# Kernel optimization log

Hardware: AMD Instinct MI355X
Metric: run time of the kernel (lower is better)

## Reference

```python
import jax, jax.numpy as jnp
import numpy as np

N = 200000      # query points
D_IN = 3        # coordinate dims
H = 256         # hidden features
L = 4           # hidden layers (between first and last Perceptron)
S = 8           # n_series == out_features


def setup_inputs() -> dict:
    key = jax.random.key(0)
    ks = jax.random.split(key, 7)
    coords = jax.random.normal(ks[0], (N, D_IN), dtype=jnp.float32)
    # Stacked per-series weights (all series share shapes; original loads the
    # same checkpoint into each, but we use independent random params).
    scale0 = 1.0 / np.sqrt(D_IN)
    scaleh = 1.0 / np.sqrt(H)
    W0 = jax.random.uniform(ks[1], (S, D_IN, H), jnp.float32, -scale0, scale0)
    b0 = jax.random.uniform(ks[2], (S, H), jnp.float32, -scale0, scale0)
    Wh = jax.random.uniform(ks[3], (S, L, H, H), jnp.float32, -scaleh, scaleh)
    bh = jax.random.uniform(ks[4], (S, L, H), jnp.float32, -scaleh, scaleh)
    Wout = jax.random.uniform(ks[5], (S, H, 1), jnp.float32, -scaleh, scaleh)
    bout = jax.random.uniform(ks[6], (S, 1), jnp.float32, -scaleh, scaleh)
    return {"coords": coords, "W0": W0, "b0": b0, "Wh": Wh, "bh": bh,
            "Wout": Wout, "bout": bout}


def reference(coords, W0, b0, Wh, bh, Wout, bout):
    # All S series' MLPs batched into grouped GEMMs (einsum over series axis s).
    # Perceptron = Linear + softplus; last layer is plain Linear.
    h = jax.nn.softplus(jnp.einsum('nd,sdh->snh', coords, W0) + b0[:, None, :])
    for i in range(L):  # small fixed layer count
        h = jax.nn.softplus(
            jnp.einsum('snh,shk->snk', h, Wh[:, i]) + bh[:, i][:, None, :])
    out = jnp.einsum('snh,sho->sno', h, Wout) + bout[:, None, :]  # [S,N,1]
    output = jnp.transpose(out[..., 0], (1, 0))  # concat along dim=1 -> [N,S]
    return (output, coords)
```

## Files before the change

### kernel.cpp

```cpp
#include <hip/hip_runtime.h>
#include <hip/hip_bf16.h>
#include <cstdint>

typedef __attribute__((ext_vector_type(8))) short short8;
typedef __attribute__((ext_vector_type(4))) float float4v;

#define LOG2E 1.44269504088896340736f
#define LN2   0.69314718055994530942f

#if __has_builtin(__builtin_amdgcn_exp2f)
__device__ __forceinline__ float fexp2(float x){ return __builtin_amdgcn_exp2f(x); }
#else
__device__ __forceinline__ float fexp2(float x){ return exp2f(x); }
#endif
#if __has_builtin(__builtin_amdgcn_logf)
__device__ __forceinline__ float flog2(float x){ return __builtin_amdgcn_logf(x); }
#else
__device__ __forceinline__ float flog2(float x){ return log2f(x); }
#endif

__device__ __forceinline__ float softplus_hat(float zh){
  return flog2(1.0f + fexp2(zh));
}

__device__ __forceinline__ unsigned short bf16_trunc(float f){
  return (unsigned short)(__builtin_bit_cast(unsigned int, f) >> 16);
}

#define HSTRIDE 264
#define MISTEP  4288
#define HSIZE   (64 * 264 + 16 * 16)

__global__ void convert_wh(const float* __restrict__ Wh,
                           unsigned short* __restrict__ Wt){
  int e = blockIdx.x * 256 + threadIdx.x;
  int n  = e & 255;
  int k  = (e >> 8) & 255;
  int sl = e >> 16;
  float v = Wh[e];
  __hip_bfloat16 h = __float2bfloat16(v);
  Wt[(sl << 16) + ((k >> 5) << 13) + (n << 5) + (k & 31)] =
      __builtin_bit_cast(unsigned short, h);
}

__device__ __forceinline__ float4v bf16_mfma(short8 a, short8 b, float4v c){
  return __builtin_amdgcn_mfma_f32_16x16x32_bf16(a, b, c, 0, 0, 0);
}

template<int L>
__device__ __forceinline__ void hidden_mfma(
    const unsigned short* __restrict__ bbase0,
    const unsigned short* __restrict__ aptr,
    short8 (&bq)[3][4], float4v (&acc)[4][4])
{
  const unsigned short* bb = bbase0 + L * 65536;
  const unsigned short* bn = bbase0 + (L + 1) * 65536;

  short8 a0[4], a1[4];
  #pragma unroll
  for (int mi = 0; mi < 4; ++mi)
    a0[mi] = *(const short8*)(aptr + mi * MISTEP);

  #pragma unroll
  for (int kb = 0; kb < 8; ++kb) {
    short8* cur = (kb & 1) ? a1 : a0;
    short8* nxt = (kb & 1) ? a0 : a1;
    if (kb < 7) {
      #pragma unroll
      for (int mi = 0; mi < 4; ++mi)
        nxt[mi] = *(const short8*)(aptr + (kb + 1) * 32 + mi * MISTEP);
    }
    const int slot = (8 * L + kb) % 3;
    #pragma unroll
    for (int mi = 0; mi < 4; ++mi)
      #pragma unroll
      for (int ni = 0; ni < 4; ++ni)
        acc[mi][ni] = bf16_mfma(cur[mi], bq[slot][ni], acc[mi][ni]);
    if (kb < 5) {
      #pragma unroll
      for (int ni = 0; ni < 4; ++ni)
        bq[slot][ni] = *(const short8*)(bb + (kb + 3) * 8192 + ni * 512);
    } else if (L < 3) {
      #pragma unroll
      for (int ni = 0; ni < 4; ++ni)
        bq[slot][ni] = *(const short8*)(bn + (kb - 5) * 8192 + ni * 512);
    }
  }
}

__global__ __launch_bounds__(256, 2) void series_mlp(
    const float* __restrict__ coords,
    const float* __restrict__ W0, const float* __restrict__ b0,
    const float* __restrict__ bh,
    const float* __restrict__ Wout, const float* __restrict__ bout,
    const unsigned short* __restrict__ Wt,
    float* __restrict__ out)
{
  __shared__ __align__(16) unsigned short h_lds[HSIZE];
  __shared__ float cbuf[192];

  const int tid  = threadIdx.x;
  const int lane = tid & 63;
  const int wave = tid >> 6;
  const int s    = blockIdx.x & 7;
  const int m0   = (blockIdx.x >> 3) * 64;

  if (tid < 192) cbuf[tid] = coords[m0 * 3 + tid];
  __syncthreads();

  {
    const int c  = tid;
    const float w0 = W0[(s * 3 + 0) * 256 + c] * LOG2E;
    const float w1 = W0[(s * 3 + 1) * 256 + c] * LOG2E;
    const float w2 = W0[(s * 3 + 2) * 256 + c] * LOG2E;
    const float bb = b0[s * 256 + c] * LOG2E;
    const float4v* c4 = (const float4v*)cbuf;
    #pragma unroll
    for (int j = 0; j < 16; ++j) {
      float4v x0 = c4[j * 3 + 0];
      float4v x1 = c4[j * 3 + 1];
      float4v x2 = c4[j * 3 + 2];
      float z0 = fmaf(x0.z, w2, fmaf(x0.y, w1, fmaf(x0.x, w0, bb)));
      float z1 = fmaf(x1.y, w2, fmaf(x1.x, w1, fmaf(x0.w, w0, bb)));
      float z2 = fmaf(x2.x, w2, fmaf(x1.w, w1, fmaf(x1.z, w0, bb)));
      float z3 = fmaf(x2.w, w2, fmaf(x2.z, w1, fmaf(x2.y, w0, bb)));
      h_lds[(4 * j + 0) * HSTRIDE + j * 16 + c] = bf16_trunc(softplus_hat(z0));
      h_lds[(4 * j + 1) * HSTRIDE + j * 16 + c] = bf16_trunc(softplus_hat(z1));
      h_lds[(4 * j + 2) * HSTRIDE + j * 16 + c] = bf16_trunc(softplus_hat(z2));
      h_lds[(4 * j + 3) * HSTRIDE + j * 16 + c] = bf16_trunc(softplus_hat(z3));
    }
  }
  __syncthreads();

  const int colb = (wave << 6) + (lane & 15);
  const int q    = lane >> 4;
  const int lr   = lane & 15;
  const unsigned short* aptr = h_lds + lr * HSTRIDE + (lr >> 2) * 16 + q * 8;
  unsigned short* cptr = h_lds + q * 1072 + colb;

  const unsigned short* bbase0 = Wt + ((s << 2) << 16) + (colb << 5) + (q << 3);

  short8 bq[3][4];
  #pragma unroll
  for (int i = 0; i < 3; ++i)
    #pragma unroll
    for (int ni = 0; ni < 4; ++ni)
      bq[i][ni] = *(const short8*)(bbase0 + i * 8192 + ni * 512);

  float4v acc[4][4];
  const float* bh_s = bh + (s << 10);

  #define HIDDEN_LAYER(L)                                                     \
  {                                                                           \
    float bias[4];                                                            \
    _Pragma("unroll")                                                         \
    for (int ni = 0; ni < 4; ++ni)                                            \
      bias[ni] = bh_s[L * 256 + colb + ni * 16] * LOG2E;                      \
    _Pragma("unroll")                                                         \
    for (int mi = 0; mi < 4; ++mi)                                            \
      _Pragma("unroll")                                                       \
      for (int ni = 0; ni < 4; ++ni)                                          \
        acc[mi][ni] = (float4v){bias[ni], bias[ni], bias[ni], bias[ni]};      \
    hidden_mfma<L>(bbase0, aptr, bq, acc);                                    \
    _Pragma("unroll")                                                         \
    for (int mi = 0; mi < 4; ++mi)                                            \
      _Pragma("unroll")                                                       \
      for (int ni = 0; ni < 4; ++ni) {                                        \
        float4v v = acc[mi][ni];                                              \
        _Pragma("unroll")                                                     \
        for (int r = 0; r < 4; ++r) v[r] = softplus_hat(v[r]);                \
        acc[mi][ni] = v;                                                      \
      }                                                                       \
    __syncthreads();                                                          \
    _Pragma("unroll")                                                         \
    for (int mi = 0; mi < 4; ++mi)                                            \
      _Pragma("unroll")                                                       \
      for (int ni = 0; ni < 4; ++ni) {                                        \
        float4v v = acc[mi][ni];                                              \
        _Pragma("unroll")                                                     \
        for (int r = 0; r < 4; ++r)                                           \
          cptr[mi * MISTEP + r * HSTRIDE + ni * 16] = bf16_trunc(v[r]);       \
      }                                                                       \
    __syncthreads();                                                          \
  }

  HIDDEN_LAYER(0)
  HIDDEN_LAYER(1)
  HIDDEN_LAYER(2)
  #undef HIDDEN_LAYER

  {
    float bias[4];
    #pragma unroll
    for (int ni = 0; ni < 4; ++ni)
      bias[ni] = bh_s[3 * 256 + colb + ni * 16] * LOG2E;
    #pragma unroll
    for (int mi = 0; mi < 4; ++mi)
      #pragma unroll
      for (int ni = 0; ni < 4; ++ni)
        acc[mi][ni] = (float4v){bias[ni], bias[ni], bias[ni], bias[ni]};

    hidden_mfma<3>(bbase0, aptr, bq, acc);

    float wv[4];
    #pragma unroll
    for (int ni = 0; ni < 4; ++ni)
      wv[ni] = Wout[(s << 8) + colb + ni * 16];
    float p[16];
    #pragma unroll
    for (int i = 0; i < 16; ++i) p[i] = 0.f;
    #pragma unroll
    for (int mi = 0; mi < 4; ++mi)
      #pragma unroll
      for (int ni = 0; ni < 4; ++ni) {
        float4v v = acc[mi][ni];
        #pragma unroll
        for (int r = 0; r < 4; ++r)
          p[mi * 4 + r] = fmaf(softplus_hat(v[r]), wv[ni], p[mi * 4 + r]);
      }

    __syncthreads();
    float* red = (float*)h_lds;
    #pragma unroll
    for (int mi = 0; mi < 4; ++mi)
      #pragma unroll
      for (int r = 0; r < 4; ++r) {
        int row = mi * 16 + (q << 2) + r;
        red[row * 68 + (wave << 4) + (lane & 15)] = p[mi * 4 + r];
      }
    __syncthreads();

    if (tid < 64) {
      const float4v* rr = (const float4v*)&red[tid * 68];
      float4v a = rr[0];
      #pragma unroll
      for (int i = 1; i < 16; ++i) {
        float4v b = rr[i];
        a.x += b.x; a.y += b.y; a.z += b.z; a.w += b.w;
      }
      float tot = (a.x + a.y) + (a.z + a.w);
      out[(m0 + tid) * 8 + s] = fmaf(LN2, tot, bout[s]);
    }
  }
}

__global__ __launch_bounds__(256) void series_mlp_slow(
    const float* __restrict__ coords,
    const float* __restrict__ W0, const float* __restrict__ b0,
    const float* __restrict__ Wh, const float* __restrict__ bh,
    const float* __restrict__ Wout, const float* __restrict__ bout,
    float* __restrict__ out)
{
  __shared__ float hh[64 * 256];
  __shared__ float cbuf[192];
  __shared__ float red[256];
  const int tid = threadIdx.x;
  const int s   = blockIdx.y;
  const int m0  = blockIdx.x * 64;

  if (tid < 192) cbuf[tid] = coords[m0 * 3 + tid];
  __syncthreads();
  {
    const float w0 = W0[(s * 3 + 0) * 256 + tid];
    const float w1 = W0[(s * 3 + 1) * 256 + tid];
    const float w2 = W0[(s * 3 + 2) * 256 + tid];
    const float bb = b0[s * 256 + tid];
    for (int m = 0; m < 64; ++m) {
      float z = fmaf(cbuf[m * 3 + 2], w2,
                fmaf(cbuf[m * 3 + 1], w1,
                fmaf(cbuf[m * 3 + 0], w0, bb)));
      hh[m * 256 + tid] = LN2 * softplus_hat(z * LOG2E);
    }
  }
  __syncthreads();

  for (int l = 0; l < 4; ++l) {
    const float* W = Wh + (((s << 2) + l) << 16);
    const float bb = bh[((s << 2) + l) * 256 + tid];
    float acc[64];
    #pragma unroll
    for (int m = 0; m < 64; ++m) acc[m] = bb;
    for (int kc = 0; kc < 64; ++kc) {
      float w0 = W[(kc * 4 + 0) * 256 + tid];
      float w1 = W[(kc * 4 + 1) * 256 + tid];
      float w2 = W[(kc * 4 + 2) * 256 + tid];
      float w3 = W[(kc * 4 + 3) * 256 + tid];
      #pragma unroll
      for (int m = 0; m < 64; ++m) {
        float4v hv = *(const float4v*)&hh[m * 256 + kc * 4];
        acc[m] = fmaf(hv.w, w3, fmaf(hv.z, w2,
                 fmaf(hv.y, w1, fmaf(hv.x, w0, acc[m]))));
      }
    }
    __syncthreads();
    #pragma unroll
    for (int m = 0; m < 64; ++m)
      hh[m * 256 + tid] = LN2 * softplus_hat(acc[m] * LOG2E);
    __syncthreads();
  }
  {
    const int m = tid >> 2, qq = tid & 3;
    const float* wv = Wout + (s << 8);
    float sum = 0.f;
    for (int i = 0; i < 16; ++i) {
      int kk = (qq << 6) + ((((tid & 15) + i) << 2) & 63);
      float4v hv = *(const float4v*)&hh[m * 256 + kk];
      sum += hv.x * wv[kk] + hv.y * wv[kk + 1] + hv.z * wv[kk + 2] + hv.w * wv[kk + 3];
    }
    red[tid] = sum;
    __syncthreads();
    if (tid < 64)
      out[(m0 + tid) * 8 + s] =
          red[tid * 4] + red[tid * 4 + 1] + red[tid * 4 + 2] + red[tid * 4 + 3] + bout[s];
  }
}

extern "C" void kernel_launch(void* const* d_in, const int* in_sizes, int n_in,
                              void* d_out, int out_size, void* d_ws, size_t ws_size,
                              hipStream_t stream) {
  const float* coords = (const float*)d_in[0];
  const float* W0     = (const float*)d_in[1];
  const float* b0     = (const float*)d_in[2];
  const float* Wh     = (const float*)d_in[3];
  const float* bh     = (const float*)d_in[4];
  const float* Wout   = (const float*)d_in[5];
  const float* bout   = (const float*)d_in[6];
  float* out = (float*)d_out;

  const size_t WT_BYTES = (size_t)8 * 4 * 256 * 256 * 2;
  if (ws_size >= WT_BYTES) {
    unsigned short* Wt = (unsigned short*)d_ws;
    convert_wh<<<8192, 256, 0, stream>>>(Wh, Wt);
    series_mlp<<<dim3(25000), dim3(256), 0, stream>>>(
        coords, W0, b0, bh, Wout, bout, Wt, out);
  } else {
    series_mlp_slow<<<dim3(3125, 8), dim3(256), 0, stream>>>(
        coords, W0, b0, Wh, bh, Wout, bout, out);
  }
  hipMemcpyAsync(out + (size_t)200000 * 8, coords,
                 (size_t)200000 * 3 * sizeof(float),
                 hipMemcpyDeviceToDevice, stream);
}
```

Before: 921.3 us.

## Split row tile into two halves and overlap softplus epilogue with next MFMA phase

```diff
diff --git a/kernel.cpp b/kernel.cpp
--- a/kernel.cpp
+++ b/kernel.cpp
@@ -4,6 +4,7 @@
 
 typedef __attribute__((ext_vector_type(8))) short short8;
 typedef __attribute__((ext_vector_type(4))) float float4v;
+typedef __attribute__((ext_vector_type(2))) unsigned int uint2v;
 
 #define LOG2E 1.44269504088896340736f
 #define LN2   0.69314718055994530942f
@@ -27,9 +28,15 @@
   return (unsigned short)(__builtin_bit_cast(unsigned int, f) >> 16);
 }
 
+__device__ __forceinline__ unsigned int bf16_pack2(float lo, float hi){
+  return __builtin_amdgcn_perm(__builtin_bit_cast(unsigned int, hi),
+                               __builtin_bit_cast(unsigned int, lo),
+                               0x07060302u);
+}
+
 #define HSTRIDE 264
 #define MISTEP  4288
-#define HSIZE   (64 * 264 + 16 * 16)
+#define TSIZE   8576
 
 __global__ void convert_wh(const float* __restrict__ Wh,
                            unsigned short* __restrict__ Wt){
@@ -47,44 +54,81 @@
   return __builtin_amdgcn_mfma_f32_16x16x32_bf16(a, b, c, 0, 0, 0);
 }
 
-template<int L>
-__device__ __forceinline__ void hidden_mfma(
-    const unsigned short* __restrict__ bbase0,
+__device__ __forceinline__ void l0_iter(
+    unsigned short* __restrict__ ht, const float4v* __restrict__ c4,
+    int j, int c, float w0, float w1, float w2, float bb)
+{
+  float4v x0 = c4[j*3+0], x1 = c4[j*3+1], x2 = c4[j*3+2];
+  float z0 = fmaf(x0.z, w2, fmaf(x0.y, w1, fmaf(x0.x, w0, bb)));
+  float z1 = fmaf(x1.y, w2, fmaf(x1.x, w1, fmaf(x0.w, w0, bb)));
+  float z2 = fmaf(x2.x, w2, fmaf(x1.w, w1, fmaf(x1.z, w0, bb)));
+  float z3 = fmaf(x2.w, w2, fmaf(x2.z, w1, fmaf(x2.y, w0, bb)));
+  ht[(4*j+0)*HSTRIDE + j*16 + c] = bf16_trunc(softplus_hat(z0));
+  ht[(4*j+1)*HSTRIDE + j*16 + c] = bf16_trunc(softplus_hat(z1));
+  ht[(4*j+2)*HSTRIDE + j*16 + c] = bf16_trunc(softplus_hat(z2));
+  ht[(4*j+3)*HSTRIDE + j*16 + c] = bf16_trunc(softplus_hat(z3));
+}
+
+__device__ __forceinline__ void sp_write(const float4v (&acc)[2][4],
+    unsigned short* __restrict__ optr, int kb)
+{
+  const int mi = kb >> 2, ni = kb & 3;
+  float4v v = acc[mi][ni];
+  float s0 = softplus_hat(v.x), s1 = softplus_hat(v.y);
+  float s2 = softplus_hat(v.z), s3 = softplus_hat(v.w);
+  uint2v dd;
+  dd.x = bf16_pack2(s0, s1);
+  dd.y = bf16_pack2(s2, s3);
+  *(uint2v*)(optr + mi*MISTEP + ni*16) = dd;
+}
+
+__device__ __forceinline__ void sp_dot(const float4v (&acc)[2][4],
+    const float4v (&wv)[4], float (&p)[2], int kb)
+{
+  const int mi = kb >> 2, ni = kb & 3;
+  float4v v = acc[mi][ni];
+  p[mi] = fmaf(softplus_hat(v.x), wv[ni].x, p[mi]);
+  p[mi] = fmaf(softplus_hat(v.y), wv[ni].y, p[mi]);
+  p[mi] = fmaf(softplus_hat(v.z), wv[ni].z, p[mi]);
+  p[mi] = fmaf(softplus_hat(v.w), wv[ni].w, p[mi]);
+}
+
+template<int PH, bool LOADN, class F>
+__device__ __forceinline__ void mfma_phase(
+    const unsigned short* __restrict__ bb,
+    const unsigned short* __restrict__ bn,
     const unsigned short* __restrict__ aptr,
-    short8 (&bq)[3][4], float4v (&acc)[4][4])
-{
-  const unsigned short* bb = bbase0 + L * 65536;
-  const unsigned short* bn = bbase0 + (L + 1) * 65536;
-
-  short8 a0[4], a1[4];
-  #pragma unroll
-  for (int mi = 0; mi < 4; ++mi)
+    short8 (&bq)[3][4], float4v (&acc)[2][4], F&& other)
+{
+  short8 a0[2], a1[2];
+  #pragma unroll
+  for (int mi = 0; mi < 2; ++mi)
     a0[mi] = *(const short8*)(aptr + mi * MISTEP);
-
   #pragma unroll
   for (int kb = 0; kb < 8; ++kb) {
     short8* cur = (kb & 1) ? a1 : a0;
     short8* nxt = (kb & 1) ? a0 : a1;
     if (kb < 7) {
       #pragma unroll
-      for (int mi = 0; mi < 4; ++mi)
+      for (int mi = 0; mi < 2; ++mi)
         nxt[mi] = *(const short8*)(aptr + (kb + 1) * 32 + mi * MISTEP);
     }
-    const int slot = (8 * L + kb) % 3;
+    const int slot = (8 * PH + kb) % 3;
     #pragma unroll
-    for (int mi = 0; mi < 4; ++mi)
+    for (int mi = 0; mi < 2; ++mi)
       #pragma unroll
       for (int ni = 0; ni < 4; ++ni)
-        acc[mi][ni] = bf16_mfma(cur[mi], bq[slot][ni], acc[mi][ni]);
+        acc[mi][ni] = bf16_mfma(bq[slot][ni], cur[mi], acc[mi][ni]);
     if (kb < 5) {
       #pragma unroll
       for (int ni = 0; ni < 4; ++ni)
         bq[slot][ni] = *(const short8*)(bb + (kb + 3) * 8192 + ni * 512);
-    } else if (L < 3) {
+    } else if (LOADN) {
       #pragma unroll
       for (int ni = 0; ni < 4; ++ni)
         bq[slot][ni] = *(const short8*)(bn + (kb - 5) * 8192 + ni * 512);
     }
+    other(kb);
   }
 }
 
@@ -96,7 +140,7 @@
     const unsigned short* __restrict__ Wt,
     float* __restrict__ out)
 {
-  __shared__ __align__(16) unsigned short h_lds[HSIZE];
+  __shared__ __align__(16) unsigned short h_lds[2 * TSIZE];
   __shared__ float cbuf[192];
 
   const int tid  = threadIdx.x;
@@ -105,41 +149,19 @@
   const int s    = blockIdx.x & 7;
   const int m0   = (blockIdx.x >> 3) * 64;
 
-  if (tid < 192) cbuf[tid] = coords[m0 * 3 + tid];
-  __syncthreads();
-
-  {
-    const int c  = tid;
-    const float w0 = W0[(s * 3 + 0) * 256 + c] * LOG2E;
-    const float w1 = W0[(s * 3 + 1) * 256 + c] * LOG2E;
-    const float w2 = W0[(s * 3 + 2) * 256 + c] * LOG2E;
-    const float bb = b0[s * 256 + c] * LOG2E;
-    const float4v* c4 = (const float4v*)cbuf;
-    #pragma unroll
-    for (int j = 0; j < 16; ++j) {
-      float4v x0 = c4[j * 3 + 0];
-      float4v x1 = c4[j * 3 + 1];
-      float4v x2 = c4[j * 3 + 2];
-      float z0 = fmaf(x0.z, w2, fmaf(x0.y, w1, fmaf(x0.x, w0, bb)));
-      float z1 = fmaf(x1.y, w2, fmaf(x1.x, w1, fmaf(x0.w, w0, bb)));
-      float z2 = fmaf(x2.x, w2, fmaf(x1.w, w1, fmaf(x1.z, w0, bb)));
-      float z3 = fmaf(x2.w, w2, fmaf(x2.z, w1, fmaf(x2.y, w0, bb)));
-      h_lds[(4 * j + 0) * HSTRIDE + j * 16 + c] = bf16_trunc(softplus_hat(z0));
-      h_lds[(4 * j + 1) * HSTRIDE + j * 16 + c] = bf16_trunc(softplus_hat(z1));
-      h_lds[(4 * j + 2) * HSTRIDE + j * 16 + c] = bf16_trunc(softplus_hat(z2));
-      h_lds[(4 * j + 3) * HSTRIDE + j * 16 + c] = bf16_trunc(softplus_hat(z3));
-    }
-  }
-  __syncthreads();
-
-  const int colb = (wave << 6) + (lane & 15);
   const int q    = lane >> 4;
   const int lr   = lane & 15;
-  const unsigned short* aptr = h_lds + lr * HSTRIDE + (lr >> 2) * 16 + q * 8;
-  unsigned short* cptr = h_lds + q * 1072 + colb;
+  const int colb = (wave << 6) + lr;
+
+  const int c = tid;
+  const float w0  = W0[(s * 3 + 0) * 256 + c] * LOG2E;
+  const float w1  = W0[(s * 3 + 1) * 256 + c] * LOG2E;
+  const float w2  = W0[(s * 3 + 2) * 256 + c] * LOG2E;
+  const float bb0 = b0[s * 256 + c] * LOG2E;
+
+  if (tid < 192) cbuf[tid] = coords[m0 * 3 + tid];
 
   const unsigned short* bbase0 = Wt + ((s << 2) << 16) + (colb << 5) + (q << 3);
-
   short8 bq[3][4];
   #pragma unroll
   for (int i = 0; i < 3; ++i)
@@ -147,101 +169,100 @@
     for (int ni = 0; ni < 4; ++ni)
       bq[i][ni] = *(const short8*)(bbase0 + i * 8192 + ni * 512);
 
-  float4v acc[4][4];
+  const unsigned short* aptrA = h_lds + lr * HSTRIDE + (lr >> 2) * 16 + (q << 3);
+  const unsigned short* aptrB = aptrA + TSIZE;
+  unsigned short* optrA = h_lds + lr * HSTRIDE + (lr >> 2) * 16 + (wave << 6) + (q << 2);
+  unsigned short* optrB = optrA + TSIZE;
+
   const float* bh_s = bh + (s << 10);
-
-  #define HIDDEN_LAYER(L)                                                     \
+  const float4v* c4 = (const float4v*)cbuf;
+
+  __syncthreads();
+  #pragma unroll
+  for (int j = 0; j < 8; ++j)
+    l0_iter(h_lds, c4, j, c, w0, w1, w2, bb0);
+  __syncthreads();
+
+  float4v accA[2][4], accB[2][4];
+
+#define INIT_ACC(ACC, LIDX)                                                   \
   {                                                                           \
-    float bias[4];                                                            \
     _Pragma("unroll")                                                         \
-    for (int ni = 0; ni < 4; ++ni)                                            \
-      bias[ni] = bh_s[L * 256 + colb + ni * 16] * LOG2E;                      \
-    _Pragma("unroll")                                                         \
-    for (int mi = 0; mi < 4; ++mi)                                            \
-      _Pragma("unroll")                                                       \
-      for (int ni = 0; ni < 4; ++ni)                                          \
-        acc[mi][ni] = (float4v){bias[ni], bias[ni], bias[ni], bias[ni]};      \
-    hidden_mfma<L>(bbase0, aptr, bq, acc);                                    \
-    _Pragma("unroll")                                                         \
-    for (int mi = 0; mi < 4; ++mi)                                            \
-      _Pragma("unroll")                                                       \
-      for (int ni = 0; ni < 4; ++ni) {                                        \
-        float4v v = acc[mi][ni];                                              \
-        _Pragma("unroll")                                                     \
-        for (int r = 0; r < 4; ++r) v[r] = softplus_hat(v[r]);                \
-        acc[mi][ni] = v;                                                      \
-      }                                                                       \
-    __syncthreads();                                                          \
-    _Pragma("unroll")                                                         \
-    for (int mi = 0; mi < 4; ++mi)                                            \
-      _Pragma("unroll")                                                       \
-      for (int ni = 0; ni < 4; ++ni) {                                        \
-        float4v v = acc[mi][ni];                                              \
-        _Pragma("unroll")                                                     \
-        for (int r = 0; r < 4; ++r)                                           \
-          cptr[mi * MISTEP + r * HSTRIDE + ni * 16] = bf16_trunc(v[r]);       \
-      }                                                                       \
-    __syncthreads();                                                          \
-  }
-
-  HIDDEN_LAYER(0)
-  HIDDEN_LAYER(1)
-  HIDDEN_LAYER(2)
-  #undef HIDDEN_LAYER
-
-  {
-    float bias[4];
-    #pragma unroll
-    for (int ni = 0; ni < 4; ++ni)
-      bias[ni] = bh_s[3 * 256 + colb + ni * 16] * LOG2E;
-    #pragma unroll
-    for (int mi = 0; mi < 4; ++mi)
-      #pragma unroll
-      for (int ni = 0; ni < 4; ++ni)
-        acc[mi][ni] = (float4v){bias[ni], bias[ni], bias[ni], bias[ni]};
-
-    hidden_mfma<3>(bbase0, aptr, bq, acc);
-
-    float wv[4];
-    #pragma unroll
-    for (int ni = 0; ni < 4; ++ni)
-      wv[ni] = Wout[(s << 8) + colb + ni * 16];
-    float p[16];
-    #pragma unroll
-    for (int i = 0; i < 16; ++i) p[i] = 0.f;
-    #pragma unroll
-    for (int mi = 0; mi < 4; ++mi)
-      #pragma unroll
-      for (int ni = 0; ni < 4; ++ni) {
-        float4v v = acc[mi][ni];
-        #pragma unroll
-        for (int r = 0; r < 4; ++r)
-          p[mi * 4 + r] = fmaf(softplus_hat(v[r]), wv[ni], p[mi * 4 + r]);
-      }
-
-    __syncthreads();
-    float* red = (float*)h_lds;
-    #pragma unroll
-    for (int mi = 0; mi < 4; ++mi)
-      #pragma unroll
-      for (int r = 0; r < 4; ++r) {
-        int row = mi * 16 + (q << 2) + r;
-        red[row * 68 + (wave << 4) + (lane & 15)] = p[mi * 4 + r];
-      }
-    __syncthreads();
-
-    if (tid < 64) {
-      const float4v* rr = (const float4v*)&red[tid * 68];
-      float4v a = rr[0];
-      #pragma unroll
-      for (int i = 1; i < 16; ++i) {
-        float4v b = rr[i];
-        a.x += b.x; a.y += b.y; a.z += b.z; a.w += b.w;
-      }
-      float tot = (a.x + a.y) + (a.z + a.w);
-      out[(m0 + tid) * 8 + s] = fmaf(LN2, tot, bout[s]);
-    }
-  }
+    for (int ni = 0; ni < 4; ++ni) {                                          \
+      float4v b4 = *(const float4v*)(bh_s + (LIDX) * 256 + (wave << 6) +      \
+                                     ni * 16 + (q << 2));                     \
+      b4.x *= LOG2E; b4.y *= LOG2E; b4.z *= LOG2E; b4.w *= LOG2E;             \
+      ACC[0][ni] = b4; ACC[1][ni] = b4;                                       \
+    }                                                                         \
+  }
+
+  INIT_ACC(accA, 0)
+  mfma_phase<0, true>(bbase0, bbase0, aptrA, bq, accA,
+      [&](int j){ l0_iter(h_lds + TSIZE, c4 + 24, j, c, w0, w1, w2, bb0); });
+  __syncthreads();
+
+  INIT_ACC(accB, 0)
+  mfma_phase<1, true>(bbase0, bbase0 + 65536, aptrB, bq, accB,
+      [&](int kb){ sp_write(accA, optrA, kb); });
+  __syncthreads();
+
+  INIT_ACC(accA, 1)
+  mfma_phase<2, true>(bbase0 + 65536, bbase0 + 65536, aptrA, bq, accA,
+      [&](int kb){ sp_write(accB, optrB, kb); });
+  __syncthreads();
+
+  INIT_ACC(accB, 1)
+  mfma_phase<3, true>(bbase0 + 65536, bbase0 + 2 * 65536, aptrB, bq, accB,
+      [&](int kb){ sp_write(accA, optrA, kb); });
+  __syncthreads();
+
+  INIT_ACC(accA, 2)
+  mfma_phase<4, true>(bbase0 + 2 * 65536, bbase0 + 2 * 65536, aptrA, bq, accA,
+      [&](int kb){ sp_write(accB, optrB, kb); });
+  __syncthreads();
+
+  INIT_ACC(accB, 2)
+  mfma_phase<5, true>(bbase0 + 2 * 65536, bbase0 + 3 * 65536, aptrB, bq, accB,
+      [&](int kb){ sp_write(accA, optrA, kb); });
+  __syncthreads();
+
+  INIT_ACC(accA, 3)
+  mfma_phase<6, true>(bbase0 + 3 * 65536, bbase0 + 3 * 65536, aptrA, bq, accA,
+      [&](int kb){ sp_write(accB, optrB, kb); });
+  __syncthreads();
+
+  INIT_ACC(accB, 3)
+  float4v wv[4];
+  #pragma unroll
+  for (int ni = 0; ni < 4; ++ni)
+    wv[ni] = *(const float4v*)(Wout + (s << 8) + (wave << 6) + ni * 16 + (q << 2));
+  float pA[2] = {0.f, 0.f}, pB[2] = {0.f, 0.f};
+
+  mfma_phase<7, false>(bbase0 + 3 * 65536, bbase0, aptrB, bq, accB,
+      [&](int kb){ sp_dot(accA, wv, pA, kb); });
+  #pragma unroll
+  for (int kb = 0; kb < 8; ++kb)
+    sp_dot(accB, wv, pB, kb);
+
+  pA[0] += __shfl_xor(pA[0], 16); pA[0] += __shfl_xor(pA[0], 32);
+  pA[1] += __shfl_xor(pA[1], 16); pA[1] += __shfl_xor(pA[1], 32);
+  pB[0] += __shfl_xor(pB[0], 16); pB[0] += __shfl_xor(pB[0], 32);
+  pB[1] += __shfl_xor(pB[1], 16); pB[1] += __shfl_xor(pB[1], 32);
+
+  float* red = (float*)h_lds;
+  if (lane < 16) {
+    red[(lr)      * 4 + wave] = pA[0];
+    red[(16 + lr) * 4 + wave] = pA[1];
+    red[(32 + lr) * 4 + wave] = pB[0];
+    red[(48 + lr) * 4 + wave] = pB[1];
+  }
+  __syncthreads();
+  if (tid < 64) {
+    float4v r4 = ((const float4v*)red)[tid];
+    float tot = (r4.x + r4.y) + (r4.z + r4.w);
+    out[(m0 + tid) * 8 + s] = fmaf(LN2, tot, bout[s]);
+  }
+#undef INIT_ACC
 }
 
 __global__ __launch_bounds__(256) void series_mlp_slow(
```

Measured after the change: 1.572 ms. 1.71x slower.
